# Kernel tuning notes

Measured on AMD Instinct MI355X. Metric: run time of the kernel, lower is better.

Reference implementation:

```python
import jax, jax.numpy as jnp
import numpy as np

N = 16384      # total nodes in batched graph
B = 64         # number of graphs (dgl.batch)
DEG = 8        # random in-degree (self-loops added on top)
C = 128        # feature width
H = 2          # heads in middle blocks
EH = 8         # E: heads of attn_seq / codebook entries
DEPTH = 2
IN = 8         # max_node_color (one-hot input width)
NE = N * DEG + N  # edges incl. self-loops


def layernorm(x, g, b, eps=1e-5):
    mu = jnp.mean(x, axis=-1, keepdims=True)
    var = jnp.mean(jnp.square(x - mu), axis=-1, keepdims=True)
    return (x - mu) * jax.lax.rsqrt(var + eps) * g + b


def gatv2(x, src, dst, Ws, bs, Wd, bd, attn):
    # DGL GATv2Conv (eval mode, attn_drop inactive, share_weights=False)
    h, c = attn.shape
    n = x.shape[0]
    el = (x @ Ws + bs).reshape(n, h, c)   # fc_src
    er = (x @ Wd + bd).reshape(n, h, c)   # fc_dst
    e = jax.nn.leaky_relu(el[src] + er[dst], negative_slope=0.2)  # [E,h,c]
    logits = jnp.einsum('ehc,hc->eh', e, attn)                    # [E,h]
    # edge softmax over incoming edges of each dst node
    m = jax.ops.segment_max(logits, dst, num_segments=n)
    a = jnp.exp(logits - m[dst])
    z = jax.ops.segment_sum(a, dst, num_segments=n)
    a = a / z[dst]
    return jax.ops.segment_sum(el[src] * a[..., None], dst, num_segments=n)  # [n,h,c]


def setup_inputs() -> dict:
    key = jax.random.key(0)
    ks = iter(jax.random.split(key, 64))
    nrm = lambda *s: jax.random.normal(next(ks), s, jnp.float32) * 0.05
    colors = jax.random.randint(next(ks), (N,), 0, IN)
    feats = jax.nn.one_hot(colors, IN, dtype=jnp.float32)
    loops = jnp.arange(N)
    src = jnp.concatenate([jax.random.randint(next(ks), (N * DEG,), 0, N), loops])
    dst = jnp.concatenate([jax.random.randint(next(ks), (N * DEG,), 0, N), loops])
    graph_ids = jnp.arange(N) // (N // B)
    inp = dict(feats=feats, src=src, dst=dst, graph_ids=graph_ids)
    # attn_up: GATv2Conv(IN -> C, 1 head)
    inp.update(up_Ws=nrm(IN, C), up_bs=nrm(C), up_Wd=nrm(IN, C), up_bd=nrm(C), up_attn=nrm(1, C))
    # depth blocks: GATv2Conv(C -> C, H heads) + ff
    inp.update(L_Ws=nrm(DEPTH, C, H * C), L_bs=nrm(DEPTH, H * C),
               L_Wd=nrm(DEPTH, C, H * C), L_bd=nrm(DEPTH, H * C),
               L_attn=nrm(DEPTH, H, C),
               ff_ln_g=jnp.ones((DEPTH, C), jnp.float32), ff_ln_b=jnp.zeros((DEPTH, C), jnp.float32),
               ff_W1=nrm(DEPTH, C, 2 * C), ff_b1=nrm(DEPTH, 2 * C),
               ff_W2=nrm(DEPTH, 2 * C, C), ff_b2=nrm(DEPTH, C),
               ff_W3=nrm(DEPTH, H * C, C), ff_b3=nrm(DEPTH, C))
    # attn_seq: GATv2Conv(C -> C, EH heads) + ff_seq
    inp.update(seq_Ws=nrm(C, EH * C), seq_bs=nrm(EH * C),
               seq_Wd=nrm(C, EH * C), seq_bd=nrm(EH * C),
               seq_attn=nrm(EH, C),
               fs_ln_g=jnp.ones((C,), jnp.float32), fs_ln_b=jnp.zeros((C,), jnp.float32),
               fs_W1=nrm(C, 2 * C), fs_b1=nrm(2 * C),
               fs_W2=nrm(2 * C, C), fs_b2=nrm(C),
               gate_W=nrm(EH * C, 1), gate_b=nrm(1))
    return inp


def reference(feats, src, dst, graph_ids,
              up_Ws, up_bs, up_Wd, up_bd, up_attn,
              L_Ws, L_bs, L_Wd, L_bd, L_attn,
              ff_ln_g, ff_ln_b, ff_W1, ff_b1, ff_W2, ff_b2, ff_W3, ff_b3,
              seq_Ws, seq_bs, seq_Wd, seq_bd, seq_attn,
              fs_ln_g, fs_ln_b, fs_W1, fs_b1, fs_W2, fs_b2,
              gate_W, gate_b):
    # attn_up (1 head) -> flatten to [N, C]
    x = gatv2(feats, src, dst, up_Ws, up_bs, up_Wd, up_bd, up_attn).reshape(N, C)
    for l in range(DEPTH):
        h = gatv2(x, src, dst, L_Ws[l], L_bs[l], L_Wd[l], L_bd[l], L_attn[l])  # [N,H,C]
        h = layernorm(h, ff_ln_g[l], ff_ln_b[l])
        h = jax.nn.gelu(h @ ff_W1[l] + ff_b1[l], approximate=False)
        h = h @ ff_W2[l] + ff_b2[l]                              # [N,H,C]
        x = h.reshape(N, H * C) @ ff_W3[l] + ff_b3[l]            # [N,C]
    y = gatv2(x, src, dst, seq_Ws, seq_bs, seq_Wd, seq_bd, seq_attn)  # [N,EH,C]
    y = layernorm(y, fs_ln_g, fs_ln_b)
    y = jax.nn.gelu(y @ fs_W1 + fs_b1, approximate=False) @ fs_W2 + fs_b2
    y = y.reshape(N, EH * C)
    # GlobalAttentionPooling: softmax(gate) over nodes within each graph
    gate = y @ gate_W + gate_b                                   # [N,1]
    gm = jax.ops.segment_max(gate, graph_ids, num_segments=B)
    ga = jnp.exp(gate - gm[graph_ids])
    gz = jax.ops.segment_sum(ga, graph_ids, num_segments=B)
    ga = ga / gz[graph_ids]
    pooled = jax.ops.segment_sum(ga * y, graph_ids, num_segments=B)  # [B, EH*C]
    return jnp.tanh(pooled.reshape(B, EH, C))
```

## Files before the change

### kernel.cpp

```cpp
#include <hip/hip_runtime.h>
#include <hip/hip_bf16.h>

typedef __hip_bfloat16 bf16;
typedef __attribute__((ext_vector_type(8))) short short8;
typedef __attribute__((ext_vector_type(4))) float f32x4;

#define NN 16384
#define NB 64
#define NE_TOT (NN*8 + NN)
#define CW 128

__device__ __forceinline__ float b2f(bf16 x){ return __bfloat162float(x); }
__device__ __forceinline__ bf16  f2b(float x){ return __float2bfloat16(x); }
__device__ __forceinline__ float lrelu(float x){ return fmaxf(x, 0.2f*x); }
__device__ __forceinline__ float gelu_f(float x){ return 0.5f*x*(1.f + erff(x*0.70710678118654752f)); }
__device__ __forceinline__ float us2f(unsigned int u){ return __uint_as_float(u << 16); }
__device__ __forceinline__ unsigned short f2us(float x){ return __builtin_bit_cast(unsigned short, f2b(x)); }

__device__ __forceinline__ void async16(const void* g, void* l){
  __builtin_amdgcn_global_load_lds((const __attribute__((address_space(1))) void*)g,
                                   (__attribute__((address_space(3))) void*)l, 16, 0, 0);
}

__global__ void k_detect(const unsigned short* __restrict__ f, int* __restrict__ flag){
  __shared__ int cnt;
  if(threadIdx.x == 0) cnt = 0;
  __syncthreads();
  int c = 0;
  for(int i = threadIdx.x; i < 2048; i += 256)
    if(f[2*i] == 0x3F80) c++;
  atomicAdd(&cnt, c);
  __syncthreads();
  if(threadIdx.x == 0) *flag = (cnt > 0) ? 0 : 1;
}

struct ConvArgs { const void* in[32]; bf16* out[32]; int n[32]; int tk[32]; int tj[32]; int ls[32]; };
__global__ __launch_bounds__(256) void k_conv_all(ConvArgs a, const int* __restrict__ flag){
  int which = blockIdx.y;
  int t = blockIdx.x*256 + threadIdx.x;
  int n = a.n[which];
  if(t >= n) return;
  float v = (*flag) ? ((const float*)a.in[which])[t] : b2f(((const bf16*)a.in[which])[t]);
  int tj = a.tj[which];
  if(tj == 0){ a.out[which][t] = f2b(v); return; }
  int tk = a.tk[which], kj = tk*tj;
  int l = t / kj, r = t - l*kj;
  int k = r / tj, j = r - k*tj;
  a.out[which][l*a.ls[which] + j*tk + k] = f2b(v);
}

__global__ void k_zero3(int* __restrict__ a, int* __restrict__ b, float* __restrict__ g, int n){
  int i = blockIdx.x*blockDim.x + threadIdx.x;
  if(i < n){ a[i] = 0; b[i] = 0; g[i] = 0.f; }
}
__global__ void k_hist(const int* __restrict__ dst, int* __restrict__ deg, int ne){
  int e = blockIdx.x*blockDim.x + threadIdx.x;
  if(e < ne) atomicAdd(&deg[dst[e]], 1);
}
__global__ void k_scan(const int* __restrict__ deg, int* __restrict__ off){
  __shared__ int s[256];
  int t = threadIdx.x;
  const int chunk = NN/256;
  int base = t*chunk;
  int sum = 0;
  for(int i=0;i<chunk;i++) sum += deg[base+i];
  s[t] = sum; __syncthreads();
  for(int o=1;o<256;o<<=1){
    int v = (t >= o) ? s[t-o] : 0;
    __syncthreads();
    s[t] += v;
    __syncthreads();
  }
  int run = (t == 0) ? 0 : s[t-1];
  for(int i=0;i<chunk;i++){ off[base+i] = run; run += deg[base+i]; }
  if(t == 255) off[NN] = run;
}
__global__ void k_scatter(const int* __restrict__ src, const int* __restrict__ dst,
                          const int* __restrict__ off, int* __restrict__ cursor,
                          int* __restrict__ csr_src, int ne){
  int e = blockIdx.x*blockDim.x + threadIdx.x;
  if(e < ne){
    int d = dst[e];
    int p = off[d] + atomicAdd(&cursor[d], 1);
    csr_src[p] = src[e];
  }
}

__global__ __launch_bounds__(128) void k_up(const bf16* __restrict__ feats,
    const bf16* __restrict__ Ws, const bf16* __restrict__ bs,
    const bf16* __restrict__ Wd, const bf16* __restrict__ bd,
    bf16* __restrict__ eler){
  int n = blockIdx.x, c = threadIdx.x;
  __shared__ float f[8];
  if(c < 8) f[c] = b2f(feats[n*8 + c]);
  __syncthreads();
  float a = b2f(bs[c]), b = b2f(bd[c]);
  #pragma unroll
  for(int k=0;k<8;k++){
    float fv = f[k];
    a += fv*b2f(Ws[k*CW + c]);
    b += fv*b2f(Wd[k*CW + c]);
  }
  eler[(size_t)n*256 + c]       = f2b(a);
  eler[(size_t)n*256 + 128 + c] = f2b(b);
}

template<int ACT>
__global__ __launch_bounds__(256) void k_mm(
    const bf16* __restrict__ A, int gshA, int gstrA,
    const bf16* __restrict__ WT, const bf16* __restrict__ bias,
    bf16* __restrict__ C, int gshC, int gstrC,
    int K, int J){
  __shared__ char smem[32768];
  short* As = (short*)smem;
  short* Bs = (short*)(smem + 16384);
  int tid = threadIdx.x, w = tid >> 6, lane = tid & 63;
  int l15 = lane & 15, q = lane >> 4;
  int wm = w >> 1, wn = w & 1;
  int bm = blockIdx.y*128, bn = blockIdx.x*128;

  f32x4 acc[4][4];
  #pragma unroll
  for(int i=0;i<4;i++)
    #pragma unroll
    for(int j=0;j<4;j++) acc[i][j] = (f32x4)0.f;

  int srow = w*32 + (lane >> 2);
  int scol = (lane & 3)*8;
  const bf16* gA[2]; const bf16* gB[2];
  short* lA[2]; short* lB[2];
  int mskA = (1 << gshA) - 1;
  #pragma unroll
  for(int a=0;a<2;a++){
    int rowA = bm + srow + a*16;
    gA[a] = A  + (size_t)(rowA >> gshA)*(size_t)gstrA + (size_t)(rowA & mskA)*K + scol;
    gB[a] = WT + (size_t)(bn + srow + a*16)*K + scol;
    lA[a] = As + (w*32 + a*16)*32;
    lB[a] = Bs + (w*32 + a*16)*32;
  }

  for(int kt=0; kt<K; kt+=64){
    #pragma unroll
    for(int a=0;a<2;a++)
      #pragma unroll
      for(int kh=0;kh<2;kh++){
        async16(gA[a] + kt + kh*32, lA[a] + kh*4096);
        async16(gB[a] + kt + kh*32, lB[a] + kh*4096);
      }
    __syncthreads();
    #pragma unroll
    for(int kh=0;kh<2;kh++){
      short8 af[4], bfr[4];
      #pragma unroll
      for(int i=0;i<4;i++) af[i]  = *(short8*)&As[kh*4096 + (wm*64 + i*16 + l15)*32 + q*8];
      #pragma unroll
      for(int j=0;j<4;j++) bfr[j] = *(short8*)&Bs[kh*4096 + (wn*64 + j*16 + l15)*32 + q*8];
      #pragma unroll
      for(int i=0;i<4;i++)
        #pragma unroll
        for(int j=0;j<4;j++)
          acc[i][j] = __builtin_amdgcn_mfma_f32_16x16x32_bf16(af[i], bfr[j], acc[i][j], 0, 0, 0);
    }
    __syncthreads();
  }

  float* ep = (float*)(smem + w*4352);
  int rr = lane >> 2;
  int cc = (lane & 3)*16;
  int mskC = (1 << gshC) - 1;
  #pragma unroll
  for(int i=0;i<4;i++){
    #pragma unroll
    for(int j=0;j<4;j++){
      float bv = b2f(bias[bn + wn*64 + j*16 + l15]);
      #pragma unroll
      for(int r=0;r<4;r++){
        float v = acc[i][j][r] + bv;
        if(ACT == 1) v = gelu_f(v);
        ep[(q*4+r)*68 + j*16 + l15] = v;
      }
    }
    float4 v0 = *(float4*)&ep[rr*68 + cc];
    float4 v1 = *(float4*)&ep[rr*68 + cc + 4];
    float4 v2 = *(float4*)&ep[rr*68 + cc + 8];
    float4 v3 = *(float4*)&ep[rr*68 + cc + 12];
    float vv[16] = {v0.x,v0.y,v0.z,v0.w, v1.x,v1.y,v1.z,v1.w,
                    v2.x,v2.y,v2.z,v2.w, v3.x,v3.y,v3.z,v3.w};
    unsigned int u[8];
    #pragma unroll
    for(int k=0;k<8;k++)
      u[k] = (unsigned int)f2us(vv[2*k]) | ((unsigned int)f2us(vv[2*k+1]) << 16);
    int row = bm + wm*64 + i*16 + rr;
    bf16* cp = C + (size_t)(row >> gshC)*(size_t)gstrC + (size_t)(row & mskC)*J + bn + wn*64 + cc;
    *(uint4*)cp       = make_uint4(u[0],u[1],u[2],u[3]);
    *(uint4*)(cp + 8) = make_uint4(u[4],u[5],u[6],u[7]);
  }
}

template<int E>
__device__ __forceinline__ void load_row(const bf16* p, float* f){
  if constexpr (E == 2){
    unsigned int v = *(const unsigned int*)p;
    f[0] = us2f(v & 0xffffu); f[1] = __uint_as_float(v & 0xffff0000u);
  } else if constexpr (E == 4){
    uint2 v = *(const uint2*)p;
    f[0] = us2f(v.x & 0xffffu); f[1] = __uint_as_float(v.x & 0xffff0000u);
    f[2] = us2f(v.y & 0xffffu); f[3] = __uint_as_float(v.y & 0xffff0000u);
  } else if constexpr (E == 8){
    uint4 a = *(const uint4*)p;
    unsigned int vs[4] = {a.x,a.y,a.z,a.w};
    #pragma unroll
    for(int i=0;i<4;i++){
      f[2*i]   = us2f(vs[i] & 0xffffu);
      f[2*i+1] = __uint_as_float(vs[i] & 0xffff0000u);
    }
  } else {
    uint4 a = *(const uint4*)p;
    uint4 b = *(const uint4*)(p + 8);
    unsigned int vs[8] = {a.x,a.y,a.z,a.w,b.x,b.y,b.z,b.w};
    #pragma unroll
    for(int i=0;i<8;i++){
      f[2*i]   = us2f(vs[i] & 0xffffu);
      f[2*i+1] = __uint_as_float(vs[i] & 0xffff0000u);
    }
  }
}
template<int E>
__device__ __forceinline__ void store_row(bf16* p, const float* f){
  unsigned int vs[E/2];
  #pragma unroll
  for(int i=0;i<E/2;i++)
    vs[i] = (unsigned int)f2us(f[2*i]) | ((unsigned int)f2us(f[2*i+1]) << 16);
  if constexpr (E == 2){ *(unsigned int*)p = vs[0]; }
  else if constexpr (E == 4){ *(uint2*)p = make_uint2(vs[0], vs[1]); }
  else if constexpr (E == 8){ *(uint4*)p = make_uint4(vs[0], vs[1], vs[2], vs[3]); }
  else {
    *(uint4*)p       = make_uint4(vs[0], vs[1], vs[2], vs[3]);
    *(uint4*)(p + 8) = make_uint4(vs[4], vs[5], vs[6], vs[7]);
  }
}

template<int GATE>
__global__ __launch_bounds__(256) void k_ff(
    const bf16* __restrict__ A, int gshA, int gstrA,
    const bf16* __restrict__ W1T, const bf16* __restrict__ b1,
    const bf16* __restrict__ W2T, const bf16* __restrict__ b2,
    bf16* __restrict__ C, int gshC, int gstrC,
    const bf16* __restrict__ gW, float* __restrict__ gate){
  __shared__ short Wb[8704];
  __shared__ short Hs[16896];
  int tid = threadIdx.x, w = tid >> 6, lane = tid & 63;
  int l15 = lane & 15, q = lane >> 4;
  int bm = blockIdx.x*64;
  int mskA = (1 << gshA) - 1, mskC = (1 << gshC) - 1;

  int rowA = bm + w*16 + l15;
  const bf16* ap = A + (size_t)(rowA >> gshA)*(size_t)gstrA + (size_t)(rowA & mskA)*128;
  short8 af[4];
  #pragma unroll
  for(int ki=0;ki<4;ki++) af[ki] = *(const short8*)&ap[ki*32 + q*8];

  for(int jt=0; jt<4; jt++){
    #pragma unroll
    for(int it=0;it<4;it++){
      int slot = tid + it*256;
      int r = slot >> 4, c8 = slot & 15;
      *(int4*)&Wb[r*132 + c8*8] = *(const int4*)&W1T[(size_t)(jt*64 + r)*128 + c8*8];
    }
    __syncthreads();
    f32x4 acc1[4] = {(f32x4)0.f, (f32x4)0.f, (f32x4)0.f, (f32x4)0.f};
    #pragma unroll
    for(int ki=0;ki<4;ki++){
      #pragma unroll
      for(int t=0;t<4;t++){
        short8 bfr = *(short8*)&Wb[(t*16 + l15)*132 + ki*32 + q*8];
        acc1[t] = __builtin_amdgcn_mfma_f32_16x16x32_bf16(af[ki], bfr, acc1[t], 0, 0, 0);
      }
    }
    #pragma unroll
    for(int t=0;t<4;t++){
      int jcol = jt*64 + t*16 + l15;
      float bv = b2f(b1[jcol]);
      #pragma unroll
      for(int r=0;r<4;r++){
        float v = gelu_f(acc1[t][r] + bv);
        Hs[(w*16 + q*4 + r)*260 + jcol] = (short)f2us(v);
      }
    }
    __syncthreads();
  }

  f32x4 acc2[8];
  #pragma unroll
  for(int t=0;t<8;t++) acc2[t] = (f32x4)0.f;
  for(int kc=0; kc<4; kc++){
    #pragma unroll
    for(int it=0;it<4;it++){
      int slot = tid + it*256;
      int r = slot >> 3, c8 = slot & 7;
      *(int4*)&Wb[r*68 + c8*8] = *(const int4*)&W2T[(size_t)r*256 + kc*64 + c8*8];
    }
    __syncthreads();
    #pragma unroll
    for(int ki=0;ki<2;ki++){
      short8 haf = *(short8*)&Hs[(w*16 + l15)*260 + kc*64 + ki*32 + q*8];
      #pragma unroll
      for(int t=0;t<8;t++){
        short8 bfr = *(short8*)&Wb[(t*16 + l15)*68 + ki*32 + q*8];
        acc2[t] = __builtin_amdgcn_mfma_f32_16x16x32_bf16(haf, bfr, acc2[t], 0, 0, 0);
      }
    }
    __syncthreads();
  }

  float* epf = (float*)Hs;
  #pragma unroll
  for(int t=0;t<8;t++){
    int jcol = t*16 + l15;
    float bv = b2f(b2[jcol]);
    #pragma unroll
    for(int r=0;r<4;r++)
      epf[(w*16 + q*4 + r)*132 + jcol] = acc2[t][r] + bv;
  }
  __syncthreads();
  int row = tid >> 2, cseg = (tid & 3)*32;
  float vv[32];
  #pragma unroll
  for(int k8=0;k8<8;k8++){
    float4 v = *(float4*)&epf[row*132 + cseg + k8*4];
    vv[k8*4+0] = v.x; vv[k8*4+1] = v.y; vv[k8*4+2] = v.z; vv[k8*4+3] = v.w;
  }
  unsigned int u[16];
  #pragma unroll
  for(int k=0;k<16;k++)
    u[k] = (unsigned int)f2us(vv[2*k]) | ((unsigned int)f2us(vv[2*k+1]) << 16);
  int rowC = bm + row;
  bf16* cpb = C + (size_t)(rowC >> gshC)*(size_t)gstrC + (size_t)(rowC & mskC)*128 + cseg;
  *(uint4*)cpb        = make_uint4(u[0], u[1], u[2], u[3]);
  *(uint4*)(cpb + 8)  = make_uint4(u[4], u[5], u[6], u[7]);
  *(uint4*)(cpb + 16) = make_uint4(u[8], u[9], u[10],u[11]);
  *(uint4*)(cpb + 24) = make_uint4(u[12],u[13],u[14],u[15]);

  if constexpr (GATE){
    float gwf[32];
    load_row<16>(gW + (rowC & 7)*128 + cseg,      gwf);
    load_row<16>(gW + (rowC & 7)*128 + cseg + 16, gwf + 16);
    float p = 0.f;
    #pragma unroll
    for(int k=0;k<32;k++) p += vv[k]*gwf[k];
    p += __shfl_xor(p, 1, 64);
    p += __shfl_xor(p, 2, 64);
    if((tid & 3) == 0) atomicAdd(&gate[rowC >> 3], p);
  }
}

template<int H, bool LNF>
__global__ __launch_bounds__(256) void k_gat(const int* __restrict__ off, const int* __restrict__ csr_src,
    const bf16* __restrict__ el, const bf16* __restrict__ er, const bf16* __restrict__ attn,
    const bf16* __restrict__ lng, const bf16* __restrict__ lnb, bf16* __restrict__ out,
    int rs_in, int rs_out){
  constexpr int EPL = 2*H;
  constexpr int G   = 64/H;
  int w = threadIdx.x >> 6, lane = threadIdx.x & 63;
  int n = blockIdx.x*4 + w;

  float ef[EPL], af[EPL];
  load_row<EPL>(er   + (size_t)n*rs_in + lane*EPL, ef);
  load_row<EPL>(attn + lane*EPL, af);

  int p0 = off[n], p1 = off[n+1];
  int deg = p1 - p0;
  int sidx = csr_src[p0 + (lane < deg ? lane : deg-1)];

  float z = 0.f;
  float acc[EPL];
  #pragma unroll
  for(int e=0;e<EPL;e++) acc[e] = 0.f;

  float xa[EPL], xb[EPL];
  {
    int s0 = __shfl(sidx, 0, 64);
    load_row<EPL>(el + (size_t)s0*rs_in + lane*EPL, xa);
  }
  if(deg > 1){
    int s1 = __shfl(sidx, 1, 64);
    load_row<EPL>(el + (size_t)s1*rs_in + lane*EPL, xb);
  }

  for(int p = 0; p < deg; p += 2){
    float na[EPL], nb[EPL];
    int i2 = p + 2, i3 = p + 3;
    int s2b = __shfl(sidx, i2 & 63, 64);
    int s3b = __shfl(sidx, i3 & 63, 64);
    if(i2 < deg){
      int sc = (i2 < 64) ? s2b : csr_src[p0 + i2];
      load_row<EPL>(el + (size_t)sc*rs_in + lane*EPL, na);
    }
    if(i3 < deg){
      int sd = (i3 < 64) ? s3b : csr_src[p0 + i3];
      load_row<EPL>(el + (size_t)sd*rs_in + lane*EPL, nb);
    }
    {
      float part = 0.f;
      #pragma unroll
      for(int e=0;e<EPL;e++) part += af[e]*lrelu(xa[e] + ef[e]);
      #pragma unroll
      for(int o=G/2; o; o>>=1) part += __shfl_xor(part, o, 64);
      float c = __expf(part);
      z += c;
      #pragma unroll
      for(int e=0;e<EPL;e++) acc[e] += c*xa[e];
    }
    if(p + 1 < deg){
      float part = 0.f;
      #pragma unroll
      for(int e=0;e<EPL;e++) part += af[e]*lrelu(xb[e] + ef[e]);
      #pragma unroll
      for(int o=G/2; o; o>>=1) part += __shfl_xor(part, o, 64);
      float c = __expf(part);
      z += c;
      #pragma unroll
      for(int e=0;e<EPL;e++) acc[e] += c*xb[e];
    }
    #pragma unroll
    for(int e=0;e<EPL;e++){ xa[e] = na[e]; xb[e] = nb[e]; }
  }
  float rz = 1.f/z;
  #pragma unroll
  for(int e=0;e<EPL;e++) acc[e] *= rz;

  if constexpr (LNF){
    float sl = 0.f;
    #pragma unroll
    for(int e=0;e<EPL;e++) sl += acc[e];
    #pragma unroll
    for(int o=G/2; o; o>>=1) sl += __shfl_xor(sl, o, 64);
    float mu = sl*(1.f/128.f);
    float qs = 0.f;
    #pragma unroll
    for(int e=0;e<EPL;e++){ float d = acc[e] - mu; qs += d*d; }
    #pragma unroll
    for(int o=G/2; o; o>>=1) qs += __shfl_xor(qs, o, 64);
    float r = rsqrtf(qs*(1.f/128.f) + 1e-5f);
    int cbase = (lane & (G-1))*EPL;
    #pragma unroll
    for(int e=0;e<EPL;e++)
      acc[e] = (acc[e] - mu)*r*b2f(lng[cbase + e]) + b2f(lnb[cbase + e]);
  }
  store_row<EPL>(out + (size_t)n*rs_out + lane*EPL, acc);
}

__global__ __launch_bounds__(64) void k_pool1(const float* __restrict__ gate,
                                              float* __restrict__ gm, float* __restrict__ gz){
  int g = blockIdx.x, lane = threadIdx.x;
  float v0 = gate[g*256 + lane], v1 = gate[g*256 + 64 + lane];
  float v2 = gate[g*256 + 128 + lane], v3 = gate[g*256 + 192 + lane];
  float m = fmaxf(fmaxf(v0,v1), fmaxf(v2,v3));
  #pragma unroll
  for(int o=32;o;o>>=1) m = fmaxf(m, __shfl_xor(m, o, 64));
  float z = __expf(v0-m) + __expf(v1-m) + __expf(v2-m) + __expf(v3-m);
  #pragma unroll
  for(int o=32;o;o>>=1) z += __shfl_xor(z, o, 64);
  if(lane == 0){ gm[g] = m; gz[g] = z; }
}

__global__ __launch_bounds__(256) void k_pool2(const float* __restrict__ gate,
    const float* __restrict__ gm, const float* __restrict__ gz,
    const bf16* __restrict__ y2, void* __restrict__ outv, const int* __restrict__ flag){
  int g = blockIdx.x >> 2, cb = blockIdx.x & 3, t = threadIdx.x;
  __shared__ float aL[256];
  aL[t] = __expf(gate[g*256 + t] - gm[g]) / gz[g];
  __syncthreads();
  int ch = cb*256 + t;
  float acc = 0.f;
  const bf16* base = y2 + (size_t)g*256*2048 + ch;
  for(int i=0;i<256;i++) acc += aL[i]*b2f(base[(size_t)i*2048]);
  float v = tanhf(acc);
  size_t idx = (size_t)g*1024 + ch;
  if(*flag) ((float*)outv)[idx] = v;
  else      ((bf16*)outv)[idx] = f2b(v);
}

extern "C" void kernel_launch(void* const* d_in, const int* in_sizes, int n_in,
                              void* d_out, int out_size, void* d_ws, size_t ws_size,
                              hipStream_t stream){
  const int* src = (const int*)d_in[1];
  const int* dst = (const int*)d_in[2];

  char* wsb = (char*)d_ws;
  size_t o = 0;
  auto take = [&](size_t bytes)->char*{
    char* p = wsb + o; o = (o + bytes + 255) & ~(size_t)255; return p;
  };
  int*   flag  = (int*)take(4);
  float* gate  = (float*)take((size_t)NN*4);
  float* gm    = (float*)take(64*4);
  float* gz    = (float*)take(64*4);
  int* deg     = (int*)take((size_t)NN*4);
  int* cursor  = (int*)take((size_t)NN*4);
  int* off     = (int*)take((size_t)(NN+1)*4);
  int* csr_src = (int*)take((size_t)NE_TOT*4);

  bf16* WcombL   = (bf16*)take((size_t)2*512*128*2);
  bf16* bcombL   = (bf16*)take((size_t)2*512*2);
  bf16* WcombSeq = (bf16*)take((size_t)2048*128*2);
  bf16* bcombSeq = (bf16*)take((size_t)2048*2);

  ConvArgs ca;
  const int fidx[32] = {0, 4,5,6,7,8, 9,10,11,12,13, 14,15,16,17,18,19,20,21,
                        22,23,24,25,26, 27,28,29,30,31,32, 33,34};
  bf16* cp[32];
  int maxn = 0;
  for(int i=0;i<32;i++){
    int n = in_sizes[fidx[i]];
    ca.in[i] = d_in[fidx[i]]; ca.n[i] = n;
    ca.tk[i] = 0; ca.tj[i] = 0; ca.ls[i] = 0;
    cp[i] = nullptr;
    if(n > maxn) maxn = n;
  }
  auto plain = [&](int i){ cp[i] = (bf16*)take((size_t)ca.n[i]*2); ca.out[i] = cp[i]; };
  auto spec  = [&](int i, bf16* dst_, int tk, int tj, int ls){
    ca.out[i] = dst_; ca.tk[i] = tk; ca.tj[i] = tj; ca.ls[i] = ls; cp[i] = dst_; };
  auto owntr = [&](int i, int tk, int tj){
    cp[i] = (bf16*)take((size_t)ca.n[i]*2);
    ca.out[i] = cp[i]; ca.tk[i] = tk; ca.tj[i] = tj; ca.ls[i] = tk*tj; };

  plain(0);
  plain(1); plain(2); plain(3); plain(4); plain(5);
  spec(6,  WcombL,          128, 256, 65536);
  spec(7,  bcombL,          256, 1,   512);
  spec(8,  WcombL + 32768,  128, 256, 65536);
  spec(9,  bcombL + 256,    256, 1,   512);
  plain(10); plain(11); plain(12);
  owntr(13, 128, 256);
  plain(14);
  owntr(15, 256, 128); plain(16);
  owntr(17, 256, 128); plain(18);
  spec(19, WcombSeq,           128, 1024, 131072);
  spec(20, bcombSeq,           1024, 1,  2048);
  spec(21, WcombSeq + 131072,  128, 1024, 131072);
  spec(22, bcombSeq + 1024,    1024, 1,  2048);
  plain(23); plain(24); plain(25);
  owntr(26, 128, 256); plain(27);
  owntr(28, 256, 128); plain(29);
  plain(30); plain(31);

  bf16* AB = (bf16*)take((size_t)NN*2048*2);
  bf16* X  = (bf16*)take((size_t)NN*128*2);
  bf16* G1 = AB + (size_t)NN*1024;
  bf16* G2 = AB + (size_t)NN*1024 + (size_t)NN*256;
  (void)ws_size; (void)n_in; (void)out_size;

  k_detect<<<1, 256, 0, stream>>>((const unsigned short*)d_in[0], flag);
  k_conv_all<<<dim3((maxn+255)/256, 32), 256, 0, stream>>>(ca, flag);

  k_zero3 <<<(NN+255)/256, 256, 0, stream>>>(deg, cursor, gate, NN);
  k_hist  <<<(NE_TOT+255)/256, 256, 0, stream>>>(dst, deg, NE_TOT);
  k_scan  <<<1, 256, 0, stream>>>(deg, off);
  k_scatter<<<(NE_TOT+255)/256, 256, 0, stream>>>(src, dst, off, cursor, csr_src, NE_TOT);

  k_up<<<NN, 128, 0, stream>>>(cp[0], cp[1], cp[2], cp[3], cp[4], AB);
  k_gat<1,false><<<NN/4, 256, 0, stream>>>(off, csr_src, AB, AB + 128, cp[5],
                                           nullptr, nullptr, X, 256, 128);

  for(int l=0; l<2; l++){
    k_mm<0><<<dim3(4, 128), 256, 0, stream>>>(X, 30, 0, WcombL + l*65536, bcombL + l*512,
                                              AB, 30, 0, 128, 512);
    k_gat<2,true><<<NN/4, 256, 0, stream>>>(off, csr_src, AB, AB + 256, cp[10] + l*256,
                                            cp[11] + l*128, cp[12] + l*128, G1, 512, 256);
    k_ff<0><<<2*NN/64, 256, 0, stream>>>(G1, 30, 0, cp[13] + l*32768, cp[14] + l*256,
                                         cp[15] + l*32768, cp[16] + l*128, G2, 30, 0,
                                         nullptr, nullptr);
    k_mm<0><<<dim3(1, 128), 256, 0, stream>>>(G2, 30, 0, cp[17] + l*32768, cp[18] + l*128,
                                              X, 30, 0, 256, 128);
  }

  k_mm<0><<<dim3(16, 128), 256, 0, stream>>>(X, 30, 0, WcombSeq, bcombSeq, AB, 30, 0, 128, 2048);
  k_gat<8,true><<<NN/4, 256, 0, stream>>>(off, csr_src, AB, AB + 1024, cp[23],
                                          cp[24], cp[25], AB + 1024, 2048, 2048);
  k_ff<1><<<131072/64, 256, 0, stream>>>(AB + 1024, 3, 2048, cp[26], cp[27],
                                         cp[28], cp[29], AB, 3, 2048,
                                         cp[30], gate);

  k_pool1<<<NB, 64, 0, stream>>>(gate, gm, gz);
  k_pool2<<<NB*4, 256, 0, stream>>>(gate, gm, gz, AB, d_out, flag);
}
```

Measured before the change: 482.6 us.

## Split each GAT node's edge loop across two wavefronts with LDS reduction

Each destination node is now processed by two wavefronts instead of one. Each wavefront handles alternating pairs of incoming edges, and the second wavefront's partial accumulators and softmax denominators are merged through shared memory. Grid size doubles to match. This targets latency-bound edge gathers by adding memory-level parallelism per node. In exchange it adds a block-wide barrier and LDS traffic, and half the wavefronts sit idle during the epilogue.

```diff
diff --git a/kernel.cpp b/kernel.cpp
--- a/kernel.cpp
+++ b/kernel.cpp
@@ -361,8 +361,12 @@
     int rs_in, int rs_out){
   constexpr int EPL = 2*H;
   constexpr int G   = 64/H;
+  constexpr int SEPL = (EPL == 16) ? 20 : EPL;
+  __shared__ float accsh[2][64][SEPL];
+  __shared__ float zsh[2][64];
   int w = threadIdx.x >> 6, lane = threadIdx.x & 63;
-  int n = blockIdx.x*4 + w;
+  int nl = w >> 1, ws = w & 1;
+  int n = blockIdx.x*2 + nl;
 
   float ef[EPL], af[EPL];
   load_row<EPL>(er   + (size_t)n*rs_in + lane*EPL, ef);
@@ -378,26 +382,26 @@
   for(int e=0;e<EPL;e++) acc[e] = 0.f;
 
   float xa[EPL], xb[EPL];
-  {
-    int s0 = __shfl(sidx, 0, 64);
-    load_row<EPL>(el + (size_t)s0*rs_in + lane*EPL, xa);
-  }
-  if(deg > 1){
-    int s1 = __shfl(sidx, 1, 64);
-    load_row<EPL>(el + (size_t)s1*rs_in + lane*EPL, xb);
-  }
-
-  for(int p = 0; p < deg; p += 2){
+  if(ws < deg){
+    int s = __shfl(sidx, ws, 64);
+    load_row<EPL>(el + (size_t)s*rs_in + lane*EPL, xa);
+  }
+  if(ws + 2 < deg){
+    int s = __shfl(sidx, ws + 2, 64);
+    load_row<EPL>(el + (size_t)s*rs_in + lane*EPL, xb);
+  }
+
+  for(int i = ws; i < deg; i += 4){
     float na[EPL], nb[EPL];
-    int i2 = p + 2, i3 = p + 3;
-    int s2b = __shfl(sidx, i2 & 63, 64);
-    int s3b = __shfl(sidx, i3 & 63, 64);
-    if(i2 < deg){
-      int sc = (i2 < 64) ? s2b : csr_src[p0 + i2];
+    int i4 = i + 4, i6 = i + 6;
+    int s4b = __shfl(sidx, i4 & 63, 64);
+    int s6b = __shfl(sidx, i6 & 63, 64);
+    if(i4 < deg){
+      int sc = (i4 < 64) ? s4b : csr_src[p0 + i4];
       load_row<EPL>(el + (size_t)sc*rs_in + lane*EPL, na);
     }
-    if(i3 < deg){
-      int sd = (i3 < 64) ? s3b : csr_src[p0 + i3];
+    if(i6 < deg){
+      int sd = (i6 < 64) ? s6b : csr_src[p0 + i6];
       load_row<EPL>(el + (size_t)sd*rs_in + lane*EPL, nb);
     }
     {
@@ -411,7 +415,7 @@
       #pragma unroll
       for(int e=0;e<EPL;e++) acc[e] += c*xa[e];
     }
-    if(p + 1 < deg){
+    if(i + 2 < deg){
       float part = 0.f;
       #pragma unroll
       for(int e=0;e<EPL;e++) part += af[e]*lrelu(xb[e] + ef[e]);
@@ -425,6 +429,19 @@
     #pragma unroll
     for(int e=0;e<EPL;e++){ xa[e] = na[e]; xb[e] = nb[e]; }
   }
+
+  if(ws == 1){
+    #pragma unroll
+    for(int e=0;e<EPL;e++) accsh[nl][lane][e] = acc[e];
+    zsh[nl][lane] = z;
+  }
+  __syncthreads();
+  if(ws == 1) return;
+
+  #pragma unroll
+  for(int e=0;e<EPL;e++) acc[e] += accsh[nl][lane][e];
+  z += zsh[nl][lane];
+
   float rz = 1.f/z;
   #pragma unroll
   for(int e=0;e<EPL;e++) acc[e] *= rz;
@@ -560,13 +577,13 @@
   k_scatter<<<(NE_TOT+255)/256, 256, 0, stream>>>(src, dst, off, cursor, csr_src, NE_TOT);
 
   k_up<<<NN, 128, 0, stream>>>(cp[0], cp[1], cp[2], cp[3], cp[4], AB);
-  k_gat<1,false><<<NN/4, 256, 0, stream>>>(off, csr_src, AB, AB + 128, cp[5],
+  k_gat<1,false><<<NN/2, 256, 0, stream>>>(off, csr_src, AB, AB + 128, cp[5],
                                            nullptr, nullptr, X, 256, 128);
 
   for(int l=0; l<2; l++){
     k_mm<0><<<dim3(4, 128), 256, 0, stream>>>(X, 30, 0, WcombL + l*65536, bcombL + l*512,
                                               AB, 30, 0, 128, 512);
-    k_gat<2,true><<<NN/4, 256, 0, stream>>>(off, csr_src, AB, AB + 256, cp[10] + l*256,
+    k_gat<2,true><<<NN/2, 256, 0, stream>>>(off, csr_src, AB, AB + 256, cp[10] + l*256,
                                             cp[11] + l*128, cp[12] + l*128, G1, 512, 256);
     k_ff<0><<<2*NN/64, 256, 0, stream>>>(G1, 30, 0, cp[13] + l*32768, cp[14] + l*256,
                                          cp[15] + l*32768, cp[16] + l*128, G2, 30, 0,
@@ -576,7 +593,7 @@
   }
 
   k_mm<0><<<dim3(16, 128), 256, 0, stream>>>(X, 30, 0, WcombSeq, bcombSeq, AB, 30, 0, 128, 2048);
-  k_gat<8,true><<<NN/4, 256, 0, stream>>>(off, csr_src, AB, AB + 1024, cp[23],
+  k_gat<8,true><<<NN/2, 256, 0, stream>>>(off, csr_src, AB, AB + 1024, cp[23],
                                           cp[24], cp[25], AB + 1024, 2048, 2048);
   k_ff<1><<<131072/64, 256, 0, stream>>>(AB + 1024, 3, 2048, cp[26], cp[27],
                                          cp[28], cp[29], AB, 3, 2048,
```

Result: no change. 491.9 us (+1.9%).

## Fuse middle-block feed-forward and W3 projection into one MFMA kernel

Applied to the files above, without the earlier changes.

Adds a kernel that runs the FF W1+GELU, W2 and the head-merging W3 projection for a 64-row tile (32 nodes × 2 heads) entirely in LDS, writing X directly. This replaces the separate k_ff and k_mm launches and the G2 intermediate round trip through global memory for each depth layer. The cost is heavier LDS use (about 50KB per block), which may lower occupancy, plus extra syncs and weights reloaded per block.

```diff
diff --git a/kernel.cpp b/kernel.cpp
--- a/kernel.cpp
+++ b/kernel.cpp
@@ -352,6 +352,139 @@
     p += __shfl_xor(p, 2, 64);
     if((tid & 3) == 0) atomicAdd(&gate[rowC >> 3], p);
   }
+}
+
+__global__ __launch_bounds__(256) void k_ffw3(
+    const bf16* __restrict__ A,
+    const bf16* __restrict__ W1T, const bf16* __restrict__ b1,
+    const bf16* __restrict__ W2T, const bf16* __restrict__ b2,
+    const bf16* __restrict__ W3T, const bf16* __restrict__ b3,
+    bf16* __restrict__ X){
+  __shared__ short Wb[8704];
+  __shared__ short Hs[16896];
+  int tid = threadIdx.x, w = tid >> 6, lane = tid & 63;
+  int l15 = lane & 15, q = lane >> 4;
+  int bm = blockIdx.x*64;
+
+  int rowA = bm + w*16 + l15;
+  const bf16* ap = A + (size_t)rowA*128;
+  short8 af[4];
+  #pragma unroll
+  for(int ki=0;ki<4;ki++) af[ki] = *(const short8*)&ap[ki*32 + q*8];
+
+  for(int jt=0; jt<4; jt++){
+    #pragma unroll
+    for(int it=0;it<4;it++){
+      int slot = tid + it*256;
+      int r = slot >> 4, c8 = slot & 15;
+      *(int4*)&Wb[r*132 + c8*8] = *(const int4*)&W1T[(size_t)(jt*64 + r)*128 + c8*8];
+    }
+    __syncthreads();
+    f32x4 acc1[4] = {(f32x4)0.f, (f32x4)0.f, (f32x4)0.f, (f32x4)0.f};
+    #pragma unroll
+    for(int ki=0;ki<4;ki++){
+      #pragma unroll
+      for(int t=0;t<4;t++){
+        short8 bfr = *(short8*)&Wb[(t*16 + l15)*132 + ki*32 + q*8];
+        acc1[t] = __builtin_amdgcn_mfma_f32_16x16x32_bf16(af[ki], bfr, acc1[t], 0, 0, 0);
+      }
+    }
+    #pragma unroll
+    for(int t=0;t<4;t++){
+      int jcol = jt*64 + t*16 + l15;
+      float bv = b2f(b1[jcol]);
+      #pragma unroll
+      for(int r=0;r<4;r++){
+        float v = gelu_f(acc1[t][r] + bv);
+        Hs[(w*16 + q*4 + r)*260 + jcol] = (short)f2us(v);
+      }
+    }
+    __syncthreads();
+  }
+
+  f32x4 acc2[8];
+  #pragma unroll
+  for(int t=0;t<8;t++) acc2[t] = (f32x4)0.f;
+  for(int kc=0; kc<4; kc++){
+    #pragma unroll
+    for(int it=0;it<4;it++){
+      int slot = tid + it*256;
+      int r = slot >> 3, c8 = slot & 7;
+      *(int4*)&Wb[r*68 + c8*8] = *(const int4*)&W2T[(size_t)r*256 + kc*64 + c8*8];
+    }
+    __syncthreads();
+    #pragma unroll
+    for(int ki=0;ki<2;ki++){
+      short8 haf = *(short8*)&Hs[(w*16 + l15)*260 + kc*64 + ki*32 + q*8];
+      #pragma unroll
+      for(int t=0;t<8;t++){
+        short8 bfr = *(short8*)&Wb[(t*16 + l15)*68 + ki*32 + q*8];
+        acc2[t] = __builtin_amdgcn_mfma_f32_16x16x32_bf16(haf, bfr, acc2[t], 0, 0, 0);
+      }
+    }
+    __syncthreads();
+  }
+  #pragma unroll
+  for(int t=0;t<8;t++){
+    int jcol = t*16 + l15;
+    float bv = b2f(b2[jcol]);
+    #pragma unroll
+    for(int r=0;r<4;r++)
+      Wb[(w*16 + q*4 + r)*128 + jcol] = (short)f2us(acc2[t][r] + bv);
+  }
+  __syncthreads();
+
+  int mt = w >> 1, jh = w & 1;
+  short8 a3[8];
+  #pragma unroll
+  for(int c=0;c<8;c++) a3[c] = *(short8*)&Wb[(mt*16 + l15)*256 + c*32 + q*8];
+  __syncthreads();
+
+  f32x4 acc3[4] = {(f32x4)0.f, (f32x4)0.f, (f32x4)0.f, (f32x4)0.f};
+  for(int kc=0; kc<4; kc++){
+    #pragma unroll
+    for(int it=0;it<4;it++){
+      int slot = tid + it*256;
+      int r = slot >> 3, c8 = slot & 7;
+      *(int4*)&Wb[r*68 + c8*8] = *(const int4*)&W3T[(size_t)r*256 + kc*64 + c8*8];
+    }
+    __syncthreads();
+    #pragma unroll
+    for(int ki=0;ki<2;ki++){
+      short8 haf = a3[kc*2 + ki];
+      #pragma unroll
+      for(int t=0;t<4;t++){
+        short8 bfr = *(short8*)&Wb[(jh*64 + t*16 + l15)*68 + ki*32 + q*8];
+        acc3[t] = __builtin_amdgcn_mfma_f32_16x16x32_bf16(haf, bfr, acc3[t], 0, 0, 0);
+      }
+    }
+    __syncthreads();
+  }
+
+  float* epf = (float*)Hs;
+  #pragma unroll
+  for(int t=0;t<4;t++){
+    int jcol = jh*64 + t*16 + l15;
+    float bv = b2f(b3[jcol]);
+    #pragma unroll
+    for(int r=0;r<4;r++)
+      epf[(mt*16 + q*4 + r)*132 + jcol] = acc3[t][r] + bv;
+  }
+  __syncthreads();
+  int row = tid >> 3, cseg = (tid & 7)*16;
+  float4 v0 = *(float4*)&epf[row*132 + cseg];
+  float4 v1 = *(float4*)&epf[row*132 + cseg + 4];
+  float4 v2 = *(float4*)&epf[row*132 + cseg + 8];
+  float4 v3 = *(float4*)&epf[row*132 + cseg + 12];
+  float vv[16] = {v0.x,v0.y,v0.z,v0.w, v1.x,v1.y,v1.z,v1.w,
+                  v2.x,v2.y,v2.z,v2.w, v3.x,v3.y,v3.z,v3.w};
+  unsigned int u[8];
+  #pragma unroll
+  for(int k=0;k<8;k++)
+    u[k] = (unsigned int)f2us(vv[2*k]) | ((unsigned int)f2us(vv[2*k+1]) << 16);
+  bf16* xp = X + (size_t)(bm/2 + row)*128 + cseg;
+  *(uint4*)xp       = make_uint4(u[0],u[1],u[2],u[3]);
+  *(uint4*)(xp + 8) = make_uint4(u[4],u[5],u[6],u[7]);
 }
 
 template<int H, bool LNF>
@@ -548,7 +681,6 @@
   bf16* AB = (bf16*)take((size_t)NN*2048*2);
   bf16* X  = (bf16*)take((size_t)NN*128*2);
   bf16* G1 = AB + (size_t)NN*1024;
-  bf16* G2 = AB + (size_t)NN*1024 + (size_t)NN*256;
   (void)ws_size; (void)n_in; (void)out_size;
 
   k_detect<<<1, 256, 0, stream>>>((const unsigned short*)d_in[0], flag);
@@ -568,11 +700,9 @@
                                               AB, 30, 0, 128, 512);
     k_gat<2,true><<<NN/4, 256, 0, stream>>>(off, csr_src, AB, AB + 256, cp[10] + l*256,
                                             cp[11] + l*128, cp[12] + l*128, G1, 512, 256);
-    k_ff<0><<<2*NN/64, 256, 0, stream>>>(G1, 30, 0, cp[13] + l*32768, cp[14] + l*256,
-                                         cp[15] + l*32768, cp[16] + l*128, G2, 30, 0,
-                                         nullptr, nullptr);
-    k_mm<0><<<dim3(1, 128), 256, 0, stream>>>(G2, 30, 0, cp[17] + l*32768, cp[18] + l*128,
-                                              X, 30, 0, 256, 128);
+    k_ffw3<<<2*NN/64, 256, 0, stream>>>(G1, cp[13] + l*32768, cp[14] + l*256,
+                                        cp[15] + l*32768, cp[16] + l*128,
+                                        cp[17] + l*32768, cp[18] + l*128, X);
   }
 
   k_mm<0><<<dim3(16, 128), 256, 0, stream>>>(X, 30, 0, WcombSeq, bcombSeq, AB, 30, 0, 128, 2048);
```

Measured after the change: 470.7 us. 1.03x faster.
